# Kernel optimization log

Measured on AMD Instinct MI355X. Metric: run time of the kernel, lower is better.

## Reference

```python
import jax, jax.numpy as jnp
import numpy as np

NUM_HEADS = 16
HEAD_DIM = 64  # hidden_size / num_heads


def setup_inputs() -> dict:
    key = jax.random.key(0)
    ks = jax.random.split(key, 20)
    B, S, H, K = 16, 1024, 1024, 64
    d = {"hidden_states": jax.random.normal(ks[0], (B, S, H), jnp.float32)}
    i = 1
    for p in ("q", "k", "v", "o"):
        d["W" + p] = jax.random.normal(ks[i], (H, H), jnp.float32) * (1.0 / np.sqrt(H)); i += 1
        d["b" + p] = jax.random.normal(ks[i], (H,), jnp.float32) * 0.02; i += 1
        d["LM" + p] = jax.random.normal(ks[i], (H, K), jnp.float32) * (1.0 / np.sqrt(K)); i += 1
        d["RM" + p] = jax.random.normal(ks[i], (K, H), jnp.float32) * (1.0 / np.sqrt(H)); i += 1
        d["F" + p] = jnp.ones((H,), jnp.float32)
    d["task"] = 0
    return d


def _proj(x, W, b, LM, RM, F):
    # RG weight reconstruction: weight = LM @ RM + W  (task==0 branch)
    w = LM @ RM + W  # [h_out, h_in]
    y = jnp.einsum("bsi,oi->bso", x, w) + b
    return y * F  # SFG per-channel scaling


def reference(hidden_states, Wq, bq, LMq, RMq, Fq, Wk, bk, LMk, RMk, Fk,
              Wv, bv, LMv, RMv, Fv, Wo, bo, LMo, RMo, Fo, task):
    B, S, H = hidden_states.shape
    nh, hd = NUM_HEADS, HEAD_DIM
    q = _proj(hidden_states, Wq, bq, LMq, RMq, Fq).reshape(B, S, nh, hd)
    k = _proj(hidden_states, Wk, bk, LMk, RMk, Fk).reshape(B, S, nh, hd)
    v = _proj(hidden_states, Wv, bv, LMv, RMv, Fv).reshape(B, S, nh, hd)
    scores = jnp.einsum("bqhd,bkhd->bhqk", q, k) / np.sqrt(hd).astype(np.float32)
    probs = jax.nn.softmax(scores, axis=-1)  # attn_dropout rate = 0.0
    ctx = jnp.einsum("bhqk,bkhd->bqhd", probs, v).reshape(B, S, H)
    out = _proj(ctx, Wo, bo, LMo, RMo, Fo)  # proj_dropout rate = 0.0
    return out
```

## Files before the change

### kernel.cpp

```cpp
#include <hip/hip_runtime.h>
#include <cstdint>
#include <cstddef>

typedef short short8 __attribute__((ext_vector_type(8)));
typedef float f32x4 __attribute__((ext_vector_type(4)));
typedef unsigned short us4 __attribute__((ext_vector_type(4)));

__device__ __forceinline__ unsigned short f2bf(float f) {
  unsigned int u = __float_as_uint(f);
  unsigned int r = (u + 0x7fffu + ((u >> 16) & 1u)) >> 16;
  return (unsigned short)r;
}
__device__ __forceinline__ float exp2_fast(float x) {
  return __builtin_amdgcn_exp2f(x);
}
__device__ __forceinline__ unsigned int cvt_pk_bf16(float a, float b) {
  unsigned int d;
  asm("v_cvt_pk_bf16_f32 %0, %1, %2" : "=v"(d) : "v"(a), "v"(b));
  return d;
}
__device__ __forceinline__ void gload_lds16(const void* g, void* l) {
  auto gp = reinterpret_cast<const __attribute__((address_space(1))) char*>(
      reinterpret_cast<uintptr_t>(g));
  auto lp = reinterpret_cast<__attribute__((address_space(3))) char*>(
      reinterpret_cast<uintptr_t>(l));
  __builtin_amdgcn_global_load_lds(gp, lp, 16, 0, 0);
}

__global__ __launch_bounds__(256) void prep_weights(
    const float* __restrict__ W, const float* __restrict__ bias,
    const float* __restrict__ LM, const float* __restrict__ RM,
    const float* __restrict__ F, float scale,
    unsigned short* __restrict__ Wout, float* __restrict__ bout) {
  const int o = blockIdx.x;
  const int tid = threadIdx.x;
  __shared__ float lm[64];
  if (tid < 64) lm[tid] = LM[o * 64 + tid];
  __syncthreads();
  const float f = F[o] * scale;
#pragma unroll
  for (int j = 0; j < 4; ++j) {
    const int i = tid + j * 256;
    float acc = W[o * 1024 + i];
#pragma unroll 16
    for (int k = 0; k < 64; ++k) acc = fmaf(lm[k], RM[k * 1024 + i], acc);
    Wout[o * 1024 + i] = f2bf(acc * f);
  }
  if (tid == 0) bout[o] = bias[o] * f;
}

__global__ __launch_bounds__(256) void cast_x(const float* __restrict__ x,
                                              unsigned short* __restrict__ y, int n4) {
  const int i = blockIdx.x * 256 + threadIdx.x;
  if (i >= n4) return;
  f32x4 v = *(const f32x4*)(x + (size_t)i * 4);
  us4 o;
  o[0] = f2bf(v[0]); o[1] = f2bf(v[1]); o[2] = f2bf(v[2]); o[3] = f2bf(v[3]);
  *(us4*)(y + (size_t)i * 4) = o;
}

template <int MODE>
__global__ __launch_bounds__(256) void gemm_bt(const unsigned short* __restrict__ A,
                                               const unsigned short* __restrict__ Bw,
                                               const float* __restrict__ bias,
                                               void* __restrict__ Cout,
                                               int M, int N, int K) {
  __shared__ unsigned short sA[128 * 64];
  __shared__ unsigned short sB[128 * 64];
  const int tid = threadIdx.x;
  const int w = tid >> 6;
  const int lane = tid & 63;
  const int quad = lane >> 4;
  const int ln = lane & 15;
  const int bm = blockIdx.x, bn = blockIdx.y;
  const int wm = w >> 1, wn = w & 1;

  f32x4 acc[4][4];
#pragma unroll
  for (int a = 0; a < 4; ++a)
#pragma unroll
    for (int b = 0; b < 4; ++b) acc[a][b] = (f32x4){0.f, 0.f, 0.f, 0.f};

  const size_t Kb = (size_t)K * 2;
  const char* Agb = (const char*)A + (size_t)bm * 128 * Kb;
  const char* Bgb = (const char*)Bw + (size_t)bn * 128 * Kb;
  char* sAb = (char*)sA;
  char* sBb = (char*)sB;
  const int sw = ln & 7;

  for (int k0 = 0; k0 < K; k0 += 64) {
    __syncthreads();
#pragma unroll
    for (int i = 0; i < 4; ++i) {
      const int Lb = w * 4096 + i * 1024 + lane * 16;
      const int r = Lb >> 7;
      const int c = (Lb >> 4) & 7;
      const int cb = ((c ^ (r & 7)) * 16);
      gload_lds16(Agb + (size_t)r * Kb + (size_t)k0 * 2 + cb, sAb + Lb);
      gload_lds16(Bgb + (size_t)r * Kb + (size_t)k0 * 2 + cb, sBb + Lb);
    }
    __syncthreads();
#pragma unroll
    for (int kk = 0; kk < 2; ++kk) {
      short8 af[4], bfv[4];
#pragma unroll
      for (int t = 0; t < 4; ++t) {
        const int ch = ((kk * 4 + quad) ^ sw) * 16;
        af[t]  = *(const short8*)(sAb + (wm * 64 + t * 16 + ln) * 128 + ch);
        bfv[t] = *(const short8*)(sBb + (wn * 64 + t * 16 + ln) * 128 + ch);
      }
#pragma unroll
      for (int mt = 0; mt < 4; ++mt)
#pragma unroll
        for (int nt = 0; nt < 4; ++nt)
          acc[mt][nt] = __builtin_amdgcn_mfma_f32_16x16x32_bf16(af[mt], bfv[nt], acc[mt][nt], 0, 0, 0);
    }
  }

  if (MODE == 0) {
    unsigned short* out = (unsigned short*)Cout;
#pragma unroll
    for (int mt = 0; mt < 4; ++mt) {
#pragma unroll
      for (int nt = 0; nt < 4; ++nt) {
        const int gn = bn * 128 + wn * 64 + nt * 16 + ln;
        const float bv = bias[gn];
        const int pidx = gn >> 10, rem = gn & 1023;
        const int hh = rem >> 6, dd = rem & 63;
        const int gm0 = bm * 128 + wm * 64 + mt * 16 + quad * 4;
        const int bb = gm0 >> 10, ss0 = gm0 & 1023;
        if (pidx < 2) {
#pragma unroll
          for (int r = 0; r < 4; ++r) {
            const size_t off = ((((size_t)pidx * 16 + bb) * 16 + hh) * 1024 + (ss0 + r)) * 64 + dd;
            out[off] = f2bf(acc[mt][nt][r] + bv);
          }
        } else {
          us4 pk;
#pragma unroll
          for (int r = 0; r < 4; ++r) pk[r] = f2bf(acc[mt][nt][r] + bv);
          const size_t off = (size_t)2 * 16777216 +
                             (((size_t)(bb * 16 + hh) * 64 + dd) * 1024 + ss0);
          *(us4*)(out + off) = pk;
        }
      }
    }
  } else {
    float* out = (float*)Cout;
#pragma unroll
    for (int mt = 0; mt < 4; ++mt) {
#pragma unroll
      for (int nt = 0; nt < 4; ++nt) {
        const int gn = bn * 128 + wn * 64 + nt * 16 + ln;
        const float bv = bias[gn];
#pragma unroll
        for (int r = 0; r < 4; ++r) {
          const int gm = bm * 128 + wm * 64 + mt * 16 + quad * 4 + r;
          out[(size_t)gm * N + gn] = acc[mt][nt][r] + bv;
        }
      }
    }
  }
}

__global__ __launch_bounds__(256) void attn(const unsigned short* __restrict__ Qb,
                                            const unsigned short* __restrict__ Kb_,
                                            const unsigned short* __restrict__ VTb,
                                            unsigned short* __restrict__ ctx) {
  __shared__ unsigned short sK[2][64 * 64];
  __shared__ unsigned short sVT[2][64 * 64];
  __shared__ unsigned short sP[128 * 72];
  const int tid = threadIdx.x;
  const int w = tid >> 6, lane = tid & 63, quad = lane >> 4, ln = lane & 15;
  const int bid = blockIdx.x;
  const int xcd = bid & 7, qt = (bid >> 3) & 7, sbh = bid >> 6;
  const int bh = xcd * 32 + sbh;
  const int b = bh >> 4, h = bh & 15;

  char* sPb = (char*)sP;
  const int sw = ln & 7;

  short8 bq[2][2];
#pragma unroll
  for (int s = 0; s < 2; ++s) {
    const unsigned short* Qg =
        Qb + ((size_t)bh * 1024 + (size_t)qt * 128 + w * 32 + s * 16 + ln) * 64;
    bq[s][0] = *(const short8*)(Qg + quad * 8);
    bq[s][1] = *(const short8*)(Qg + 32 + quad * 8);
  }

  f32x4 accO[2][4];
#pragma unroll
  for (int s = 0; s < 2; ++s)
#pragma unroll
    for (int nt = 0; nt < 4; ++nt) accO[s][nt] = (f32x4){0.f, 0.f, 0.f, 0.f};
  float mrun[2] = {-3e38f, -3e38f}, lrun[2] = {0.f, 0.f};

  const char* Kbase = (const char*)Kb_ + (size_t)bh * 131072;
  const char* Vbase = (const char*)VTb + (size_t)bh * 131072;

  auto stage = [&](int kt, int buf) {
#pragma unroll
    for (int i = 0; i < 2; ++i) {
      const int Lb = w * 2048 + i * 1024 + lane * 16;
      const int r = Lb >> 7;
      const int c = (Lb >> 4) & 7;
      const int cb = ((c ^ (r & 7)) * 16);
      gload_lds16(Kbase + (size_t)kt * 8192 + (size_t)r * 128 + cb, (char*)sK[buf] + Lb);
      gload_lds16(Vbase + (size_t)kt * 128 + (size_t)r * 2048 + cb, (char*)sVT[buf] + Lb);
    }
  };

  stage(0, 0);

  for (int kt = 0; kt < 16; ++kt) {
    const int cur = kt & 1;
    char* sKb = (char*)sK[cur];
    char* sVb = (char*)sVT[cur];

    stage((kt + 1) & 15, cur ^ 1);
    asm volatile("s_waitcnt vmcnt(4)" ::: "memory");
    __builtin_amdgcn_s_barrier();
    asm volatile("" ::: "memory");

    f32x4 accS[2][4];
#pragma unroll
    for (int s = 0; s < 2; ++s)
#pragma unroll
      for (int mt = 0; mt < 4; ++mt) accS[s][mt] = (f32x4){0.f, 0.f, 0.f, 0.f};
#pragma unroll
    for (int kk = 0; kk < 2; ++kk) {
      short8 ak[4];
#pragma unroll
      for (int mt = 0; mt < 4; ++mt)
        ak[mt] = *(const short8*)(sKb + (mt * 16 + ln) * 128 + ((kk * 4 + quad) ^ sw) * 16);
      __builtin_amdgcn_s_setprio(1);
#pragma unroll
      for (int s = 0; s < 2; ++s)
#pragma unroll
        for (int mt = 0; mt < 4; ++mt)
          accS[s][mt] = __builtin_amdgcn_mfma_f32_16x16x32_bf16(ak[mt], bq[s][kk], accS[s][mt], 0, 0, 0);
      __builtin_amdgcn_s_setprio(0);
    }

#pragma unroll
    for (int s = 0; s < 2; ++s) {
      float tmax = -3e38f;
#pragma unroll
      for (int mt = 0; mt < 4; ++mt)
#pragma unroll
        for (int r = 0; r < 4; ++r) tmax = fmaxf(tmax, accS[s][mt][r]);
      tmax = fmaxf(tmax, __shfl_xor(tmax, 16));
      tmax = fmaxf(tmax, __shfl_xor(tmax, 32));
      if (!__all(tmax <= mrun[s] + 8.0f)) {
        const float mnew = fmaxf(mrun[s], tmax);
        const float alpha = exp2_fast(mrun[s] - mnew);
        mrun[s] = mnew;
        lrun[s] *= alpha;
#pragma unroll
        for (int r = 0; r < 4; ++r) {
          const float ar = __shfl(alpha, quad * 4 + r);
#pragma unroll
          for (int nt = 0; nt < 4; ++nt) accO[s][nt][r] *= ar;
        }
      }
      const float m = mrun[s];
      float psum = 0.f;
#pragma unroll
      for (int mt = 0; mt < 4; ++mt) {
        float p0 = exp2_fast(accS[s][mt][0] - m);
        float p1 = exp2_fast(accS[s][mt][1] - m);
        float p2 = exp2_fast(accS[s][mt][2] - m);
        float p3 = exp2_fast(accS[s][mt][3] - m);
        psum += (p0 + p1) + (p2 + p3);
        union { unsigned int u[2]; us4 v; } pu;
        pu.u[0] = cvt_pk_bf16(p0, p1);
        pu.u[1] = cvt_pk_bf16(p2, p3);
        *(us4*)(sP + (w * 32 + s * 16 + ln) * 72 + mt * 16 + quad * 4) = pu.v;
      }
      lrun[s] += psum;
    }

    asm volatile("" ::: "memory");

#pragma unroll
    for (int kk = 0; kk < 2; ++kk) {
      short8 ap[2];
#pragma unroll
      for (int s = 0; s < 2; ++s)
        ap[s] = *(const short8*)(sPb + (w * 32 + s * 16 + ln) * 144 + kk * 64 + quad * 16);
#pragma unroll
      for (int nt = 0; nt < 4; ++nt) {
        const short8 bv = *(const short8*)(sVb + (nt * 16 + ln) * 128 + ((kk * 4 + quad) ^ sw) * 16);
        __builtin_amdgcn_s_setprio(1);
#pragma unroll
        for (int s = 0; s < 2; ++s)
          accO[s][nt] = __builtin_amdgcn_mfma_f32_16x16x32_bf16(ap[s], bv, accO[s][nt], 0, 0, 0);
        __builtin_amdgcn_s_setprio(0);
      }
    }

    __builtin_amdgcn_s_barrier();
    asm volatile("" ::: "memory");
  }

#pragma unroll
  for (int s = 0; s < 2; ++s) {
    float l = lrun[s];
    l += __shfl_xor(l, 16);
    l += __shfl_xor(l, 32);
    const float inv = 1.0f / l;
#pragma unroll
    for (int r = 0; r < 4; ++r) {
      const float ivr = __shfl(inv, quad * 4 + r);
      const int sg = qt * 128 + w * 32 + s * 16 + quad * 4 + r;
#pragma unroll
      for (int nt = 0; nt < 4; ++nt) {
        const int d = nt * 16 + ln;
        ctx[((size_t)(b * 1024 + sg)) * 1024 + h * 64 + d] = f2bf(accO[s][nt][r] * ivr);
      }
    }
  }
}

extern "C" void kernel_launch(void* const* d_in, const int* in_sizes, int n_in,
                              void* d_out, int out_size, void* d_ws, size_t ws_size,
                              hipStream_t stream) {
  const float* hs  = (const float*)d_in[0];
  const float* Wq  = (const float*)d_in[1];
  const float* bq  = (const float*)d_in[2];
  const float* LMq = (const float*)d_in[3];
  const float* RMq = (const float*)d_in[4];
  const float* Fq  = (const float*)d_in[5];
  const float* Wk  = (const float*)d_in[6];
  const float* bk  = (const float*)d_in[7];
  const float* LMk = (const float*)d_in[8];
  const float* RMk = (const float*)d_in[9];
  const float* Fk  = (const float*)d_in[10];
  const float* Wv  = (const float*)d_in[11];
  const float* bv  = (const float*)d_in[12];
  const float* LMv = (const float*)d_in[13];
  const float* RMv = (const float*)d_in[14];
  const float* Fv  = (const float*)d_in[15];
  const float* Wo  = (const float*)d_in[16];
  const float* bo  = (const float*)d_in[17];
  const float* LMo = (const float*)d_in[18];
  const float* RMo = (const float*)d_in[19];
  const float* Fo  = (const float*)d_in[20];

  char* p = (char*)d_ws;
  unsigned short* xbf  = (unsigned short*)p; p += (size_t)16384 * 1024 * 2;
  unsigned short* Wqkv = (unsigned short*)p; p += (size_t)3072 * 1024 * 2;
  unsigned short* Wob  = (unsigned short*)p; p += (size_t)1024 * 1024 * 2;
  float* bqkv = (float*)p; p += 3072 * 4;
  float* bob  = (float*)p; p += 1024 * 4;
  unsigned short* qkv = (unsigned short*)p; p += (size_t)3 * 16777216 * 2;
  unsigned short* ctx = (unsigned short*)p; p += (size_t)16777216 * 2;

  const float qscale = 0.125f * 1.4426950408889634f;

  cast_x<<<16384, 256, 0, stream>>>(hs, xbf, 16777216 / 4);
  prep_weights<<<1024, 256, 0, stream>>>(Wq, bq, LMq, RMq, Fq, qscale, Wqkv, bqkv);
  prep_weights<<<1024, 256, 0, stream>>>(Wk, bk, LMk, RMk, Fk, 1.0f, Wqkv + 1024 * 1024, bqkv + 1024);
  prep_weights<<<1024, 256, 0, stream>>>(Wv, bv, LMv, RMv, Fv, 1.0f, Wqkv + 2 * 1024 * 1024, bqkv + 2048);
  prep_weights<<<1024, 256, 0, stream>>>(Wo, bo, LMo, RMo, Fo, 1.0f, Wob, bob);

  gemm_bt<0><<<dim3(128, 24), 256, 0, stream>>>(xbf, Wqkv, bqkv, (void*)qkv, 16384, 3072, 1024);

  attn<<<2048, 256, 0, stream>>>(qkv, qkv + 16777216, qkv + 2 * 16777216, ctx);

  gemm_bt<1><<<dim3(128, 8), 256, 0, stream>>>(ctx, Wob, bob, d_out, 16384, 1024, 1024);
}
```

Before: 485.9 us.

## Switch attention to 32x32x16 MFMA and keep P in registers via permlane swap

Rewrites the attention kernel's S=K·Q^T and O=P·V products to use 32x32x16 bf16 MFMA instead of 16x16x32. The probability tile is converted to bf16 and rearranged across lane halves with v_permlane32_swap, so it feeds the PV MFMA directly from registers and the sP shared-memory round trip is removed. This cuts LDS traffic and shuffles in the softmax. It changes the accumulator layout and the output write pattern, and adds correctness risk in the lane mapping.

```diff
diff --git a/kernel.cpp b/kernel.cpp
--- a/kernel.cpp
+++ b/kernel.cpp
@@ -4,6 +4,7 @@
 
 typedef short short8 __attribute__((ext_vector_type(8)));
 typedef float f32x4 __attribute__((ext_vector_type(4)));
+typedef float f32x16 __attribute__((ext_vector_type(16)));
 typedef unsigned short us4 __attribute__((ext_vector_type(4)));
 
 __device__ __forceinline__ unsigned short f2bf(float f) {
@@ -18,6 +19,9 @@
   unsigned int d;
   asm("v_cvt_pk_bf16_f32 %0, %1, %2" : "=v"(d) : "v"(a), "v"(b));
   return d;
+}
+__device__ __forceinline__ void permlane32_swap2(unsigned int& a, unsigned int& b) {
+  asm("v_permlane32_swap_b32 %0, %1" : "+v"(a), "+v"(b));
 }
 __device__ __forceinline__ void gload_lds16(const void* g, void* l) {
   auto gp = reinterpret_cast<const __attribute__((address_space(1))) char*>(
@@ -169,32 +173,29 @@
                                             unsigned short* __restrict__ ctx) {
   __shared__ unsigned short sK[2][64 * 64];
   __shared__ unsigned short sVT[2][64 * 64];
-  __shared__ unsigned short sP[128 * 72];
   const int tid = threadIdx.x;
-  const int w = tid >> 6, lane = tid & 63, quad = lane >> 4, ln = lane & 15;
+  const int w = tid >> 6, lane = tid & 63;
+  const int col = lane & 31, hi = lane >> 5;
+  const int sw7 = col & 7;
   const int bid = blockIdx.x;
   const int xcd = bid & 7, qt = (bid >> 3) & 7, sbh = bid >> 6;
   const int bh = xcd * 32 + sbh;
   const int b = bh >> 4, h = bh & 15;
 
-  char* sPb = (char*)sP;
-  const int sw = ln & 7;
-
-  short8 bq[2][2];
-#pragma unroll
-  for (int s = 0; s < 2; ++s) {
+  short8 bq[4];
+  {
     const unsigned short* Qg =
-        Qb + ((size_t)bh * 1024 + (size_t)qt * 128 + w * 32 + s * 16 + ln) * 64;
-    bq[s][0] = *(const short8*)(Qg + quad * 8);
-    bq[s][1] = *(const short8*)(Qg + 32 + quad * 8);
-  }
-
-  f32x4 accO[2][4];
-#pragma unroll
-  for (int s = 0; s < 2; ++s)
-#pragma unroll
-    for (int nt = 0; nt < 4; ++nt) accO[s][nt] = (f32x4){0.f, 0.f, 0.f, 0.f};
-  float mrun[2] = {-3e38f, -3e38f}, lrun[2] = {0.f, 0.f};
+        Qb + ((size_t)bh * 1024 + (size_t)qt * 128 + w * 32 + col) * 64 + hi * 8;
+#pragma unroll
+    for (int ks = 0; ks < 4; ++ks) bq[ks] = *(const short8*)(Qg + ks * 16);
+  }
+
+  f32x16 accO[2];
+#pragma unroll
+  for (int nt = 0; nt < 2; ++nt)
+#pragma unroll
+    for (int r = 0; r < 16; ++r) accO[nt][r] = 0.f;
+  float mrun = -3e38f, lrun = 0.f;
 
   const char* Kbase = (const char*)Kb_ + (size_t)bh * 131072;
   const char* Vbase = (const char*)VTb + (size_t)bh * 131072;
@@ -215,111 +216,99 @@
 
   for (int kt = 0; kt < 16; ++kt) {
     const int cur = kt & 1;
-    char* sKb = (char*)sK[cur];
-    char* sVb = (char*)sVT[cur];
+    const char* sKb = (const char*)sK[cur];
+    const char* sVb = (const char*)sVT[cur];
 
     stage((kt + 1) & 15, cur ^ 1);
     asm volatile("s_waitcnt vmcnt(4)" ::: "memory");
     __builtin_amdgcn_s_barrier();
     asm volatile("" ::: "memory");
 
-    f32x4 accS[2][4];
-#pragma unroll
-    for (int s = 0; s < 2; ++s)
-#pragma unroll
-      for (int mt = 0; mt < 4; ++mt) accS[s][mt] = (f32x4){0.f, 0.f, 0.f, 0.f};
-#pragma unroll
-    for (int kk = 0; kk < 2; ++kk) {
-      short8 ak[4];
-#pragma unroll
-      for (int mt = 0; mt < 4; ++mt)
-        ak[mt] = *(const short8*)(sKb + (mt * 16 + ln) * 128 + ((kk * 4 + quad) ^ sw) * 16);
+    f32x16 accS[2];
+#pragma unroll
+    for (int mt = 0; mt < 2; ++mt)
+#pragma unroll
+      for (int r = 0; r < 16; ++r) accS[mt][r] = 0.f;
+#pragma unroll
+    for (int ks = 0; ks < 4; ++ks) {
+      const int ch = (((2 * ks + hi) ^ sw7) * 16);
+      const short8 ak0 = *(const short8*)(sKb + (col)*128 + ch);
+      const short8 ak1 = *(const short8*)(sKb + (32 + col) * 128 + ch);
       __builtin_amdgcn_s_setprio(1);
-#pragma unroll
-      for (int s = 0; s < 2; ++s)
-#pragma unroll
-        for (int mt = 0; mt < 4; ++mt)
-          accS[s][mt] = __builtin_amdgcn_mfma_f32_16x16x32_bf16(ak[mt], bq[s][kk], accS[s][mt], 0, 0, 0);
+      accS[0] = __builtin_amdgcn_mfma_f32_32x32x16_bf16(ak0, bq[ks], accS[0], 0, 0, 0);
+      accS[1] = __builtin_amdgcn_mfma_f32_32x32x16_bf16(ak1, bq[ks], accS[1], 0, 0, 0);
       __builtin_amdgcn_s_setprio(0);
     }
 
-#pragma unroll
-    for (int s = 0; s < 2; ++s) {
-      float tmax = -3e38f;
-#pragma unroll
-      for (int mt = 0; mt < 4; ++mt)
-#pragma unroll
-        for (int r = 0; r < 4; ++r) tmax = fmaxf(tmax, accS[s][mt][r]);
-      tmax = fmaxf(tmax, __shfl_xor(tmax, 16));
-      tmax = fmaxf(tmax, __shfl_xor(tmax, 32));
-      if (!__all(tmax <= mrun[s] + 8.0f)) {
-        const float mnew = fmaxf(mrun[s], tmax);
-        const float alpha = exp2_fast(mrun[s] - mnew);
-        mrun[s] = mnew;
-        lrun[s] *= alpha;
-#pragma unroll
-        for (int r = 0; r < 4; ++r) {
-          const float ar = __shfl(alpha, quad * 4 + r);
-#pragma unroll
-          for (int nt = 0; nt < 4; ++nt) accO[s][nt][r] *= ar;
-        }
-      }
-      const float m = mrun[s];
-      float psum = 0.f;
-#pragma unroll
-      for (int mt = 0; mt < 4; ++mt) {
-        float p0 = exp2_fast(accS[s][mt][0] - m);
-        float p1 = exp2_fast(accS[s][mt][1] - m);
-        float p2 = exp2_fast(accS[s][mt][2] - m);
-        float p3 = exp2_fast(accS[s][mt][3] - m);
-        psum += (p0 + p1) + (p2 + p3);
-        union { unsigned int u[2]; us4 v; } pu;
-        pu.u[0] = cvt_pk_bf16(p0, p1);
-        pu.u[1] = cvt_pk_bf16(p2, p3);
-        *(us4*)(sP + (w * 32 + s * 16 + ln) * 72 + mt * 16 + quad * 4) = pu.v;
-      }
-      lrun[s] += psum;
-    }
-
-    asm volatile("" ::: "memory");
-
-#pragma unroll
-    for (int kk = 0; kk < 2; ++kk) {
-      short8 ap[2];
-#pragma unroll
-      for (int s = 0; s < 2; ++s)
-        ap[s] = *(const short8*)(sPb + (w * 32 + s * 16 + ln) * 144 + kk * 64 + quad * 16);
-#pragma unroll
-      for (int nt = 0; nt < 4; ++nt) {
-        const short8 bv = *(const short8*)(sVb + (nt * 16 + ln) * 128 + ((kk * 4 + quad) ^ sw) * 16);
+    float tmax = -3e38f;
+#pragma unroll
+    for (int mt = 0; mt < 2; ++mt)
+#pragma unroll
+      for (int r = 0; r < 16; ++r) tmax = fmaxf(tmax, accS[mt][r]);
+    tmax = fmaxf(tmax, __shfl_xor(tmax, 32));
+    if (!__all(tmax <= mrun + 8.0f)) {
+      const float mnew = fmaxf(mrun, tmax);
+      const float alpha = exp2_fast(mrun - mnew);
+      mrun = mnew;
+      lrun *= alpha;
+#pragma unroll
+      for (int r = 0; r < 16; ++r) {
+        const float ar = __shfl(alpha, (r & 3) + 8 * (r >> 2) + 4 * hi);
+        accO[0][r] *= ar;
+        accO[1][r] *= ar;
+      }
+    }
+    const float m = mrun;
+
+    float psum = 0.f;
+#pragma unroll
+    for (int mt = 0; mt < 2; ++mt) {
+#pragma unroll
+      for (int c = 0; c < 2; ++c) {
+        const int r0 = c * 8;
+        const float e0 = exp2_fast(accS[mt][r0 + 0] - m);
+        const float e1 = exp2_fast(accS[mt][r0 + 1] - m);
+        const float e2 = exp2_fast(accS[mt][r0 + 2] - m);
+        const float e3 = exp2_fast(accS[mt][r0 + 3] - m);
+        const float e4 = exp2_fast(accS[mt][r0 + 4] - m);
+        const float e5 = exp2_fast(accS[mt][r0 + 5] - m);
+        const float e6 = exp2_fast(accS[mt][r0 + 6] - m);
+        const float e7 = exp2_fast(accS[mt][r0 + 7] - m);
+        psum += ((e0 + e1) + (e2 + e3)) + ((e4 + e5) + (e6 + e7));
+        unsigned int x = cvt_pk_bf16(e0, e1);
+        unsigned int y = cvt_pk_bf16(e2, e3);
+        unsigned int z = cvt_pk_bf16(e4, e5);
+        unsigned int t = cvt_pk_bf16(e6, e7);
+        permlane32_swap2(x, z);
+        permlane32_swap2(y, t);
+        union { unsigned int u[4]; short8 v; } pa;
+        pa.u[0] = x; pa.u[1] = y; pa.u[2] = z; pa.u[3] = t;
+        const int cs = mt * 4 + c * 2 + hi;
+        const int ch = ((cs ^ sw7) * 16);
+        const short8 bv0 = *(const short8*)(sVb + (col)*128 + ch);
+        const short8 bv1 = *(const short8*)(sVb + (32 + col) * 128 + ch);
         __builtin_amdgcn_s_setprio(1);
-#pragma unroll
-        for (int s = 0; s < 2; ++s)
-          accO[s][nt] = __builtin_amdgcn_mfma_f32_16x16x32_bf16(ap[s], bv, accO[s][nt], 0, 0, 0);
+        accO[0] = __builtin_amdgcn_mfma_f32_32x32x16_bf16(pa.v, bv0, accO[0], 0, 0, 0);
+        accO[1] = __builtin_amdgcn_mfma_f32_32x32x16_bf16(pa.v, bv1, accO[1], 0, 0, 0);
         __builtin_amdgcn_s_setprio(0);
       }
     }
+    lrun += psum;
 
     __builtin_amdgcn_s_barrier();
     asm volatile("" ::: "memory");
   }
 
-#pragma unroll
-  for (int s = 0; s < 2; ++s) {
-    float l = lrun[s];
-    l += __shfl_xor(l, 16);
-    l += __shfl_xor(l, 32);
-    const float inv = 1.0f / l;
-#pragma unroll
-    for (int r = 0; r < 4; ++r) {
-      const float ivr = __shfl(inv, quad * 4 + r);
-      const int sg = qt * 128 + w * 32 + s * 16 + quad * 4 + r;
-#pragma unroll
-      for (int nt = 0; nt < 4; ++nt) {
-        const int d = nt * 16 + ln;
-        ctx[((size_t)(b * 1024 + sg)) * 1024 + h * 64 + d] = f2bf(accO[s][nt][r] * ivr);
-      }
-    }
+  float lt = lrun + __shfl_xor(lrun, 32);
+  const float inv = 1.0f / lt;
+#pragma unroll
+  for (int r = 0; r < 16; ++r) {
+    const int qr = (r & 3) + 8 * (r >> 2) + 4 * hi;
+    const float iv = __shfl(inv, qr);
+    const int sg = qt * 128 + w * 32 + qr;
+    const size_t base = ((size_t)(b * 1024 + sg)) * 1024 + h * 64;
+    ctx[base + col] = f2bf(accO[0][r] * iv);
+    ctx[base + 32 + col] = f2bf(accO[1][r] * iv);
   }
 }
 
```

Result: no change. 487.8 us (+0.4%).
